# Optimization experiments

Hardware: AMD Instinct MI355X
Metric: run time of the kernel (lower is better)

Reference implementation:

```python
import jax, jax.numpy as jnp
import numpy as np
from jax import lax

B, S, D = 2, 2048, 1024
DS, K, L = 16, 4, 6
DI = 2 * D          # expand * d_model
V, A = 32000, 7
EPS = 1e-5


def setup_inputs() -> dict:
    key = jax.random.key(0)
    ks = jax.random.split(key, 20)
    g = lambda i, shape, s=0.02: (jax.random.normal(ks[i], shape, dtype=jnp.float32) * s)
    return {
        "features": jax.random.normal(ks[0], (B, S, D), dtype=jnp.float32),
        # per-layer Mamba params, stacked on leading layer dim
        "in_proj_w": g(1, (L, D, 2 * DI)),
        "conv_w": g(2, (L, DI, K), 0.1),
        "conv_b": g(3, (L, DI), 0.0),
        "B_ssm": g(4, (L, DI, DS)),   # fixed analogs of the per-step torch.randn(d_inner,d_state)
        "C_ssm": g(5, (L, DS, DI)),   # fixed analogs of the per-step torch.randn(d_state,d_inner)
        "out_w": g(6, (L, DI, D)),
        "ln_g": jnp.ones((D,), jnp.float32),
        "ln_b": jnp.zeros((D,), jnp.float32),
        # action head (arm: 7-dof, bounds (-1,1))
        "act_w1": g(7, (D, D // 2)), "act_b1": jnp.zeros((D // 2,), jnp.float32),
        "act_w2": g(8, (D // 2, D // 4)), "act_b2": jnp.zeros((D // 4,), jnp.float32),
        "act_w3": g(9, (D // 4, A)), "act_b3": jnp.zeros((A,), jnp.float32),
        # language head
        "lang_w1": g(10, (D, D)), "lang_b1": jnp.zeros((D,), jnp.float32),
        "lang_w2": g(11, (D, V)), "lang_b2": jnp.zeros((V,), jnp.float32),
    }


def _causal_dwconv(x, w, b):
    # x: [B,S,DI], w: [DI,K], b: [DI]  -> causal depthwise conv (torch pad=K-1 then trim)
    lhs = x.transpose(0, 2, 1)                    # [B,DI,S]
    rhs = w[:, None, :]                           # [DI,1,K]
    y = lax.conv_general_dilated(lhs, rhs, window_strides=(1,),
                                 padding=[(K - 1, 0)], feature_group_count=DI,
                                 dimension_numbers=("NCH", "OIH", "NCH"))
    return (y + b[None, :, None]).transpose(0, 2, 1)  # [B,S,DI]


def _selective_scan(xc, Bm, Cm):
    # xc: [B,S,DI]; h_t = 0.9*h_{t-1} + (x_t @ Bm)*0.1 ; y_t = h_t @ Cm
    u = jnp.einsum("bsi,in->bsn", xc, Bm) * 0.1      # [B,S,DS]
    def step(h, u_t):
        h = 0.9 * h + u_t
        return h, h
    _, hs = lax.scan(step, jnp.zeros((xc.shape[0], DS), xc.dtype), u.transpose(1, 0, 2))
    return jnp.einsum("sbn,ni->bsi", hs, Cm)         # [B,S,DI]


def _mamba_block(x, in_w, cw, cb, Bm, Cm, ow):
    xz = jnp.einsum("bsd,do->bso", x, in_w)          # [B,S,2*DI]
    xp, z = xz[..., :DI], xz[..., DI:]
    xc = jax.nn.silu(_causal_dwconv(xp, cw, cb))
    y = _selective_scan(xc, Bm, Cm) * jax.nn.silu(z)
    return jnp.einsum("bsi,id->bsd", y, ow)


def _forward(features, in_proj_w, conv_w, conv_b, B_ssm, C_ssm, out_w,
             ln_g, ln_b, act_w1, act_b1, act_w2, act_b2, act_w3, act_b3,
             lang_w1, lang_b1, lang_w2, lang_b2):
    x = features
    for l in range(L):  # residual Mamba layers (fallback path: x = x + block(x))
        x = x + _mamba_block(x, in_proj_w[l], conv_w[l], conv_b[l],
                             B_ssm[l], C_ssm[l], out_w[l])
    mu = jnp.mean(x, -1, keepdims=True)
    var = jnp.mean(jnp.square(x - mu), -1, keepdims=True)
    x = (x - mu) * lax.rsqrt(var + EPS) * ln_g + ln_b
    # action head: bounds (-1,1) => affine rescale is identity
    h = jax.nn.relu(x @ act_w1 + act_b1)
    h = jax.nn.relu(h @ act_w2 + act_b2)
    actions = jnp.tanh(h @ act_w3 + act_b3)
    # language head
    logits = jax.nn.relu(x @ lang_w1 + lang_b1) @ lang_w2 + lang_b2
    return actions, logits


def reference(features, in_proj_w, conv_w, conv_b, B_ssm, C_ssm, out_w,
              ln_g, ln_b, act_w1, act_b1, act_w2, act_b2, act_w3, act_b3,
              lang_w1, lang_b1, lang_w2, lang_b2):
    return _forward(features, in_proj_w, conv_w, conv_b, B_ssm, C_ssm, out_w,
                    ln_g, ln_b, act_w1, act_b1, act_w2, act_b2, act_w3, act_b3,
                    lang_w1, lang_b1, lang_w2, lang_b2)
```

## Files before the change

kernel.cpp:

```cpp
#include <hip/hip_runtime.h>
#include <hip/hip_bf16.h>
#include <cstdint>
#include <cstddef>

#define TT 4096
#define SS 2048
#define DD 1024
#define DDI 2048
#define LL 6
#define VV 32000
#define AA 7

typedef __hip_bfloat16 bf16;
typedef __attribute__((ext_vector_type(8))) short bf16x8;
typedef __attribute__((ext_vector_type(4))) short bf16x4;
typedef __attribute__((ext_vector_type(4))) float f32x4;

typedef const __attribute__((address_space(1))) void* gas_ptr;
typedef __attribute__((address_space(3))) void* las_ptr;

static __device__ __forceinline__ float b2f(bf16 h) { return __bfloat162float(h); }
static __device__ __forceinline__ bf16 f2b(float f) { return __float2bfloat16(f); }
static __device__ __forceinline__ float bs2f(short x) {
    unsigned int u = ((unsigned int)(unsigned short)x) << 16;
    float f; __builtin_memcpy(&f, &u, 4); return f;
}
static __device__ __forceinline__ short f2bs(float f) {
    bf16 h = f2b(f); unsigned short us; __builtin_memcpy(&us, &h, 2); return (short)us;
}

#define SWZ(off) ((off) ^ ((((off) >> 7) & 3) << 4))

template<int EPI>
__global__ __launch_bounds__(512, 2)
void g8_k(const bf16* __restrict__ A, const bf16* __restrict__ Wt,
          int K, int mx, int out_ld,
          float* __restrict__ of32, bf16* __restrict__ ob16,
          const float* __restrict__ bias)
{
    extern __shared__ char lds[];
    const int nwg = gridDim.x;
    int l = blockIdx.x;
    if ((nwg & 7) == 0) l = (l & 7) * (nwg >> 3) + (l >> 3);
    const int row0 = (l % mx) * 256, col0 = (l / mx) * 256;

    const int tid = threadIdx.x, wid = tid >> 6, lane = tid & 63;
    const int wr = wid >> 2, wc = wid & 3;
    const int l15 = lane & 15, kq = lane >> 4;

    f32x4 acc[8][4];
#pragma unroll
    for (int m = 0; m < 8; ++m)
#pragma unroll
        for (int n = 0; n < 4; ++n) acc[m][n] = f32x4{0.f, 0.f, 0.f, 0.f};

    const int sr   = tid >> 2;
    const int colE = (((tid & 3) ^ ((tid >> 3) & 3)) * 8);
    const bf16* gA = A  + (size_t)(row0 + sr) * K + colE;
    const bf16* gB = Wt + (size_t)(col0 + sr) * K + colE;
    const int dst0 = tid * 16, dst1 = 8192 + tid * 16;

    auto stageA = [&](int kh) {
        char* b = lds + (kh & 3) * 16384;
        __builtin_amdgcn_global_load_lds((gas_ptr)(gA + kh * 32),                   (las_ptr)(b + dst0), 16, 0, 0);
        __builtin_amdgcn_global_load_lds((gas_ptr)(gA + (size_t)128 * K + kh * 32), (las_ptr)(b + dst1), 16, 0, 0);
    };
    auto stageB = [&](int kh) {
        char* b = lds + 65536 + (kh & 3) * 16384;
        __builtin_amdgcn_global_load_lds((gas_ptr)(gB + kh * 32),                   (las_ptr)(b + dst0), 16, 0, 0);
        __builtin_amdgcn_global_load_lds((gas_ptr)(gB + (size_t)128 * K + kh * 32), (las_ptr)(b + dst1), 16, 0, 0);
    };

    const int NT = K >> 6, KH = K >> 5;
    stageA(0); stageB(0); stageA(1); stageB(1);
    stageA(2); stageB(2); stageA(3); stageB(3);
    int nextA = 4, nextB = 4;

    for (int t = 0; t < NT; ++t) {
        const char* As0 = lds + ((2 * t) & 3) * 16384;
        const char* As1 = lds + ((2 * t + 1) & 3) * 16384;
        const char* Bs0 = lds + 65536 + ((2 * t) & 3) * 16384;
        const char* Bs1 = lds + 65536 + ((2 * t + 1) & 3) * 16384;
        bf16x8 af[4], bfg[4];

        if (t < NT - 3) asm volatile("s_waitcnt vmcnt(10)" ::: "memory");
        else            asm volatile("s_waitcnt vmcnt(0)" ::: "memory");
        __builtin_amdgcn_sched_barrier(0);
        __builtin_amdgcn_s_barrier();
        __builtin_amdgcn_sched_barrier(0);
#pragma unroll
        for (int fn = 0; fn < 4; ++fn)
            bfg[fn] = *(const bf16x8*)(Bs0 + SWZ((wc * 64 + fn * 16 + l15) * 64 + kq * 16));
#pragma unroll
        for (int fm = 0; fm < 4; ++fm)
            af[fm] = *(const bf16x8*)(As0 + SWZ((wr * 128 + fm * 16 + l15) * 64 + kq * 16));
        if (t > 0 && nextA < KH) { stageA(nextA); ++nextA; }
        asm volatile("s_waitcnt lgkmcnt(0)" ::: "memory");
        __builtin_amdgcn_sched_barrier(0);
        __builtin_amdgcn_s_setprio(1);
#pragma unroll
        for (int fm = 0; fm < 4; ++fm)
#pragma unroll
            for (int fn = 0; fn < 4; ++fn)
                acc[fm][fn] = __builtin_amdgcn_mfma_f32_16x16x32_bf16(af[fm], bfg[fn], acc[fm][fn], 0, 0, 0);
        __builtin_amdgcn_s_setprio(0);
        __builtin_amdgcn_sched_barrier(0);
        __builtin_amdgcn_s_barrier();
        __builtin_amdgcn_sched_barrier(0);

#pragma unroll
        for (int fm = 0; fm < 4; ++fm)
            af[fm] = *(const bf16x8*)(As0 + SWZ((wr * 128 + 64 + fm * 16 + l15) * 64 + kq * 16));
        if (nextB < KH) { stageB(nextB); ++nextB; }
        asm volatile("s_waitcnt lgkmcnt(0)" ::: "memory");
        __builtin_amdgcn_sched_barrier(0);
        __builtin_amdgcn_s_setprio(1);
#pragma unroll
        for (int fm = 0; fm < 4; ++fm)
#pragma unroll
            for (int fn = 0; fn < 4; ++fn)
                acc[4 + fm][fn] = __builtin_amdgcn_mfma_f32_16x16x32_bf16(af[fm], bfg[fn], acc[4 + fm][fn], 0, 0, 0);
        __builtin_amdgcn_s_setprio(0);
        __builtin_amdgcn_sched_barrier(0);
        __builtin_amdgcn_s_barrier();
        __builtin_amdgcn_sched_barrier(0);

        if (t < NT - 3) asm volatile("s_waitcnt vmcnt(10)" ::: "memory");
        else            asm volatile("s_waitcnt vmcnt(0)" ::: "memory");
        __builtin_amdgcn_sched_barrier(0);
        __builtin_amdgcn_s_barrier();
        __builtin_amdgcn_sched_barrier(0);
#pragma unroll
        for (int fn = 0; fn < 4; ++fn)
            bfg[fn] = *(const bf16x8*)(Bs1 + SWZ((wc * 64 + fn * 16 + l15) * 64 + kq * 16));
#pragma unroll
        for (int fm = 0; fm < 4; ++fm)
            af[fm] = *(const bf16x8*)(As1 + SWZ((wr * 128 + fm * 16 + l15) * 64 + kq * 16));
        if (nextA < KH) { stageA(nextA); ++nextA; }
        asm volatile("s_waitcnt lgkmcnt(0)" ::: "memory");
        __builtin_amdgcn_sched_barrier(0);
        __builtin_amdgcn_s_setprio(1);
#pragma unroll
        for (int fm = 0; fm < 4; ++fm)
#pragma unroll
            for (int fn = 0; fn < 4; ++fn)
                acc[fm][fn] = __builtin_amdgcn_mfma_f32_16x16x32_bf16(af[fm], bfg[fn], acc[fm][fn], 0, 0, 0);
        __builtin_amdgcn_s_setprio(0);
        __builtin_amdgcn_sched_barrier(0);
        __builtin_amdgcn_s_barrier();
        __builtin_amdgcn_sched_barrier(0);

#pragma unroll
        for (int fm = 0; fm < 4; ++fm)
            af[fm] = *(const bf16x8*)(As1 + SWZ((wr * 128 + 64 + fm * 16 + l15) * 64 + kq * 16));
        if (nextB < KH) { stageB(nextB); ++nextB; }
        asm volatile("s_waitcnt lgkmcnt(0)" ::: "memory");
        __builtin_amdgcn_sched_barrier(0);
        __builtin_amdgcn_s_setprio(1);
#pragma unroll
        for (int fm = 0; fm < 4; ++fm)
#pragma unroll
            for (int fn = 0; fn < 4; ++fn)
                acc[4 + fm][fn] = __builtin_amdgcn_mfma_f32_16x16x32_bf16(af[fm], bfg[fn], acc[4 + fm][fn], 0, 0, 0);
        __builtin_amdgcn_s_setprio(0);
        __builtin_amdgcn_sched_barrier(0);
        __builtin_amdgcn_s_barrier();
        __builtin_amdgcn_sched_barrier(0);
    }

    float* sc = (float*)(lds + wid * 16384);
#pragma unroll
    for (int h = 0; h < 2; ++h) {
        asm volatile("s_waitcnt lgkmcnt(0)" ::: "memory");
        __builtin_amdgcn_sched_barrier(0);
#pragma unroll
        for (int fm = 0; fm < 4; ++fm)
#pragma unroll
            for (int fn = 0; fn < 4; ++fn)
#pragma unroll
                for (int r = 0; r < 4; ++r)
                    sc[(fm * 16 + kq * 4 + r) * 64 + fn * 16 + l15] = acc[h * 4 + fm][fn][r];
        asm volatile("s_waitcnt lgkmcnt(0)" ::: "memory");
        __builtin_amdgcn_sched_barrier(0);
#pragma unroll
        for (int j = 0; j < 16; ++j) {
            const int rl = j * 4 + kq;
            f32x4 v4 = *(const f32x4*)&sc[rl * 64 + l15 * 4];
            const int row = row0 + wr * 128 + h * 64 + rl;
            const int col = col0 + wc * 64 + l15 * 4;
            if (EPI == 0) {
                bf16x4 ov = { f2bs(v4[0]), f2bs(v4[1]), f2bs(v4[2]), f2bs(v4[3]) };
                *(bf16x4*)(ob16 + (size_t)row * out_ld + col) = ov;
            } else {
                float4 bv = *(const float4*)(bias + col);
                f32x4 ov = { v4[0] + bv.x, v4[1] + bv.y, v4[2] + bv.z, v4[3] + bv.w };
                *(f32x4*)(of32 + (size_t)row * out_ld + col) = ov;
            }
        }
    }
}

template<int EPI>
__global__ __launch_bounds__(256, 2)
void g8h_k(const bf16* __restrict__ A, const bf16* __restrict__ Wt,
           int K, int mx, int out_ld,
           float* __restrict__ of32, bf16* __restrict__ ob16,
           const float* __restrict__ bias)
{
    extern __shared__ char lds[];
    const int nwg = gridDim.x;
    int l = blockIdx.x;
    if ((nwg & 7) == 0) l = (l & 7) * (nwg >> 3) + (l >> 3);
    const int row0 = (l % mx) * 128, col0 = (l / mx) * 128;

    const int tid = threadIdx.x, wid = tid >> 6, lane = tid & 63;
    const int wr = wid >> 1, wc = wid & 1;
    const int l15 = lane & 15, kq = lane >> 4;

    f32x4 acc[4][4];
#pragma unroll
    for (int m = 0; m < 4; ++m)
#pragma unroll
        for (int n = 0; n < 4; ++n) acc[m][n] = f32x4{0.f, 0.f, 0.f, 0.f};

    const int sr   = tid >> 2;
    const int colE = (((tid & 3) ^ ((tid >> 3) & 3)) * 8);
    const bf16* gA = A  + (size_t)(row0 + sr) * K + colE;
    const bf16* gB = Wt + (size_t)(col0 + sr) * K + colE;
    const int dst0 = tid * 16, dst1 = 4096 + tid * 16;

    auto stage = [&](int kh) {
        char* a = lds + (kh % 5) * 8192;
        char* b = lds + 40960 + (kh % 5) * 8192;
        __builtin_amdgcn_global_load_lds((gas_ptr)(gA + kh * 32),                  (las_ptr)(a + dst0), 16, 0, 0);
        __builtin_amdgcn_global_load_lds((gas_ptr)(gA + (size_t)64 * K + kh * 32), (las_ptr)(a + dst1), 16, 0, 0);
        __builtin_amdgcn_global_load_lds((gas_ptr)(gB + kh * 32),                  (las_ptr)(b + dst0), 16, 0, 0);
        __builtin_amdgcn_global_load_lds((gas_ptr)(gB + (size_t)64 * K + kh * 32), (las_ptr)(b + dst1), 16, 0, 0);
    };

    const int KH = K >> 5;
    stage(0); stage(1); stage(2); stage(3);

    for (int kh = 0; kh < KH; ++kh) {
        const int rem = KH - 1 - kh;
        if (rem >= 3)      asm volatile("s_waitcnt vmcnt(12)" ::: "memory");
        else if (rem == 2) asm volatile("s_waitcnt vmcnt(8)" ::: "memory");
        else if (rem == 1) asm volatile("s_waitcnt vmcnt(4)" ::: "memory");
        else               asm volatile("s_waitcnt vmcnt(0)" ::: "memory");
        __builtin_amdgcn_sched_barrier(0);
        __builtin_amdgcn_s_barrier();
        __builtin_amdgcn_sched_barrier(0);

        const char* As = lds + (kh % 5) * 8192;
        const char* Bs = lds + 40960 + (kh % 5) * 8192;
        bf16x8 af[4], bfg[4];
#pragma unroll
        for (int fn = 0; fn < 4; ++fn)
            bfg[fn] = *(const bf16x8*)(Bs + SWZ((wc * 64 + fn * 16 + l15) * 64 + kq * 16));
#pragma unroll
        for (int fm = 0; fm < 4; ++fm)
            af[fm] = *(const bf16x8*)(As + SWZ((wr * 64 + fm * 16 + l15) * 64 + kq * 16));
        if (kh + 4 < KH) stage(kh + 4);
        asm volatile("s_waitcnt lgkmcnt(0)" ::: "memory");
        __builtin_amdgcn_sched_barrier(0);
        __builtin_amdgcn_s_setprio(1);
#pragma unroll
        for (int fm = 0; fm < 4; ++fm)
#pragma unroll
            for (int fn = 0; fn < 4; ++fn)
                acc[fm][fn] = __builtin_amdgcn_mfma_f32_16x16x32_bf16(af[fm], bfg[fn], acc[fm][fn], 0, 0, 0);
        __builtin_amdgcn_s_setprio(0);
        __builtin_amdgcn_sched_barrier(0);
    }

#pragma unroll
    for (int fm = 0; fm < 4; ++fm) {
#pragma unroll
        for (int fn = 0; fn < 4; ++fn) {
#pragma unroll
            for (int r = 0; r < 4; ++r) {
                const int row = row0 + wr * 64 + fm * 16 + kq * 4 + r;
                const int col = col0 + wc * 64 + fn * 16 + l15;
                float v = acc[fm][fn][r];
                if (EPI == 3) {
                    float rr = of32[(size_t)row * out_ld + col] + v;
                    of32[(size_t)row * out_ld + col] = rr;
                    ob16[(size_t)row * out_ld + col] = f2b(rr);
                } else {
                    ob16[(size_t)row * out_ld + col] = f2b(v);
                }
            }
        }
    }
}

template<int EPI>
__global__ __launch_bounds__(256)
void gemm_k(const bf16* __restrict__ A, const bf16* __restrict__ Wt,
            int K, int out_ld,
            float* __restrict__ of32, bf16* __restrict__ ob16,
            const float* __restrict__ bias)
{
    __shared__ bf16x8 lsA8[128 * 4];
    __shared__ bf16x8 lsB8[128 * 4];
    bf16* lsA = (bf16*)lsA8;
    bf16* lsB = (bf16*)lsB8;

    const int tid  = threadIdx.x;
    const int w    = tid >> 6;
    const int lane = tid & 63;
    const int row0 = blockIdx.x * 128;
    const int col0 = blockIdx.y * 128;
    const int wr   = (w >> 1) * 64;
    const int wc   = (w & 1) * 64;
    const int l15  = lane & 15;
    const int kq   = lane >> 4;

    f32x4 acc[4][4];
#pragma unroll
    for (int m = 0; m < 4; ++m)
#pragma unroll
        for (int n = 0; n < 4; ++n) acc[m][n] = f32x4{0.f, 0.f, 0.f, 0.f};

    const int s0 = tid, s1 = tid + 256;
    const size_t ga0 = (size_t)(row0 + (s0 >> 2)) * K + (s0 & 3) * 8;
    const size_t ga1 = (size_t)(row0 + (s1 >> 2)) * K + (s1 & 3) * 8;
    const size_t gb0 = (size_t)(col0 + (s0 >> 2)) * K + (s0 & 3) * 8;
    const size_t gb1 = (size_t)(col0 + (s1 >> 2)) * K + (s1 & 3) * 8;
    bf16* la0 = lsA + (size_t)(w * 64) * 8;
    bf16* la1 = lsA + (size_t)(256 + w * 64) * 8;
    bf16* lb0 = lsB + (size_t)(w * 64) * 8;
    bf16* lb1 = lsB + (size_t)(256 + w * 64) * 8;

    for (int k0 = 0; k0 < K; k0 += 32) {
        __builtin_amdgcn_global_load_lds((gas_ptr)(A  + ga0 + k0), (las_ptr)la0, 16, 0, 0);
        __builtin_amdgcn_global_load_lds((gas_ptr)(A  + ga1 + k0), (las_ptr)la1, 16, 0, 0);
        __builtin_amdgcn_global_load_lds((gas_ptr)(Wt + gb0 + k0), (las_ptr)lb0, 16, 0, 0);
        __builtin_amdgcn_global_load_lds((gas_ptr)(Wt + gb1 + k0), (las_ptr)lb1, 16, 0, 0);
        __syncthreads();

        bf16x8 af[4], bfr[4];
#pragma unroll
        for (int m = 0; m < 4; ++m)
            af[m] = *(const bf16x8*)(lsA + (size_t)(wr + m * 16 + l15) * 32 + kq * 8);
#pragma unroll
        for (int n = 0; n < 4; ++n)
            bfr[n] = *(const bf16x8*)(lsB + (size_t)(wc + n * 16 + l15) * 32 + kq * 8);
#pragma unroll
        for (int m = 0; m < 4; ++m)
#pragma unroll
            for (int n = 0; n < 4; ++n)
                acc[m][n] = __builtin_amdgcn_mfma_f32_16x16x32_bf16(af[m], bfr[n], acc[m][n], 0, 0, 0);
        __syncthreads();
    }

#pragma unroll
    for (int m = 0; m < 4; ++m) {
#pragma unroll
        for (int n = 0; n < 4; ++n) {
#pragma unroll
            for (int r = 0; r < 4; ++r) {
                const int row = row0 + wr + m * 16 + kq * 4 + r;
                const int col = col0 + wc + n * 16 + l15;
                float v = acc[m][n][r];
                v = fmaxf(v + bias[col], 0.f);
                ob16[(size_t)row * out_ld + col] = f2b(v);
            }
        }
    }
}

__global__ __launch_bounds__(256)
void cusk_k(const bf16* __restrict__ xz, const float* __restrict__ cw,
            const float* __restrict__ cb, const bf16* __restrict__ Wt,
            float* __restrict__ up)
{
    __shared__ bf16x8 lsA8[128 * 4];
    __shared__ bf16x8 lsB8[128 * 4];
    bf16* lsA = (bf16*)lsA8;
    bf16* lsB = (bf16*)lsB8;
    const int K = 2048;

    const int tid  = threadIdx.x;
    const int w    = tid >> 6;
    const int lane = tid & 63;
    const int row0 = blockIdx.x * 128;
    const int spl  = blockIdx.y;
    const int kbeg = spl * 256;
    const int wr   = (w >> 1) * 64;
    const int wc   = (w & 1) * 64;
    const int l15  = lane & 15;
    const int kq   = lane >> 4;

    f32x4 acc[4][4];
#pragma unroll
    for (int m = 0; m < 4; ++m)
#pragma unroll
        for (int n = 0; n < 4; ++n) acc[m][n] = f32x4{0.f, 0.f, 0.f, 0.f};

    const int trow = tid >> 2, tch = tid & 3;
    const int r0g = row0 + trow, r1g = r0g + 64;
    const int sq0 = r0g & (SS - 1), sq1 = r1g & (SS - 1);

    const int s0 = tid, s1 = tid + 256;
    const size_t gb0 = (size_t)(s0 >> 2) * K + (s0 & 3) * 8;
    const size_t gb1 = (size_t)(s1 >> 2) * K + (s1 & 3) * 8;
    bf16* lb0 = lsB + (size_t)(w * 64) * 8;
    bf16* lb1 = lsB + (size_t)(256 + w * 64) * 8;

    for (int k0 = kbeg; k0 < kbeg + 256; k0 += 32) {
        const int i0 = k0 + tch * 8;

        __builtin_amdgcn_global_load_lds((gas_ptr)(Wt + gb0 + k0), (las_ptr)lb0, 16, 0, 0);
        __builtin_amdgcn_global_load_lds((gas_ptr)(Wt + gb1 + k0), (las_ptr)lb1, 16, 0, 0);

        bf16x8 vA0, vA1;
        {
            const bf16* b0 = xz + (size_t)r0g * 4096 + i0;
            bf16x8 x0 = *(const bf16x8*)b0;
            bf16x8 x1 = {}, x2 = {}, x3 = {};
            if (sq0 >= 1) x1 = *(const bf16x8*)(b0 - 4096);
            if (sq0 >= 2) x2 = *(const bf16x8*)(b0 - 2 * 4096);
            if (sq0 >= 3) x3 = *(const bf16x8*)(b0 - 3 * 4096);
#pragma unroll
            for (int c = 0; c < 8; ++c) {
                float4 wv4 = ((const float4*)cw)[i0 + c];
                float a = cb[i0 + c];
                a = fmaf(bs2f(x3[c]), wv4.x, a);
                a = fmaf(bs2f(x2[c]), wv4.y, a);
                a = fmaf(bs2f(x1[c]), wv4.z, a);
                a = fmaf(bs2f(x0[c]), wv4.w, a);
                float sig = 1.f / (1.f + expf(-a));
                vA0[c] = f2bs(a * sig);
            }
        }
        {
            const bf16* b0 = xz + (size_t)r1g * 4096 + i0;
            bf16x8 x0 = *(const bf16x8*)b0;
            bf16x8 x1 = {}, x2 = {}, x3 = {};
            if (sq1 >= 1) x1 = *(const bf16x8*)(b0 - 4096);
            if (sq1 >= 2) x2 = *(const bf16x8*)(b0 - 2 * 4096);
            if (sq1 >= 3) x3 = *(const bf16x8*)(b0 - 3 * 4096);
#pragma unroll
            for (int c = 0; c < 8; ++c) {
                float4 wv4 = ((const float4*)cw)[i0 + c];
                float a = cb[i0 + c];
                a = fmaf(bs2f(x3[c]), wv4.x, a);
                a = fmaf(bs2f(x2[c]), wv4.y, a);
                a = fmaf(bs2f(x1[c]), wv4.z, a);
                a = fmaf(bs2f(x0[c]), wv4.w, a);
                float sig = 1.f / (1.f + expf(-a));
                vA1[c] = f2bs(a * sig);
            }
        }
        lsA8[tid] = vA0;
        lsA8[tid + 256] = vA1;
        __syncthreads();

        bf16x8 af[4], bfr[4];
#pragma unroll
        for (int m = 0; m < 4; ++m)
            af[m] = *(const bf16x8*)(lsA + (size_t)(wr + m * 16 + l15) * 32 + kq * 8);
#pragma unroll
        for (int n = 0; n < 4; ++n)
            bfr[n] = *(const bf16x8*)(lsB + (size_t)(wc + n * 16 + l15) * 32 + kq * 8);
#pragma unroll
        for (int m = 0; m < 4; ++m)
#pragma unroll
            for (int n = 0; n < 4; ++n)
                acc[m][n] = __builtin_amdgcn_mfma_f32_16x16x32_bf16(af[m], bfr[n], acc[m][n], 0, 0, 0);
        __syncthreads();
    }

    if (wc == 0) {
#pragma unroll
        for (int m = 0; m < 4; ++m)
#pragma unroll
            for (int r = 0; r < 4; ++r) {
                const int row = row0 + wr + m * 16 + kq * 4 + r;
                up[(size_t)spl * TT * 16 + (size_t)row * 16 + l15] = acc[m][0][r];
            }
    }
}

__global__ void ured_k(const float* __restrict__ up, float* __restrict__ u)
{
    int i = blockIdx.x * 256 + threadIdx.x;
    float s = 0.f;
#pragma unroll
    for (int k = 0; k < 8; ++k) s += up[(size_t)k * TT * 16 + i];
    u[i] = s;
}

__global__ __launch_bounds__(256)
void transpose_k(const float* __restrict__ W, bf16* __restrict__ WT, int K, int N)
{
    __shared__ bf16 t[64][66];
    const int k0 = blockIdx.x * 64, n0 = blockIdx.y * 64;
    const int tid = threadIdx.x;
#pragma unroll
    for (int i = 0; i < 16; ++i) {
        int idx = i * 256 + tid;
        int kk = idx >> 6, nn = idx & 63;
        t[nn][kk] = f2b(W[(size_t)(k0 + kk) * N + n0 + nn]);
    }
    __syncthreads();
#pragma unroll
    for (int i = 0; i < 16; ++i) {
        int idx = i * 256 + tid;
        int nn = idx >> 6, kk = idx & 63;
        WT[(size_t)(n0 + nn) * K + k0 + kk] = t[nn][kk];
    }
}

__global__ void prep_bm_k(const float* __restrict__ Bm, bf16* __restrict__ BmT)
{
    int idx = blockIdx.x * 256 + threadIdx.x;
    int n = idx >> 11, k = idx & 2047;
    float v = (n < 16) ? Bm[(size_t)k * 16 + n] * 0.1f : 0.f;
    BmT[idx] = f2b(v);
}

__global__ void copyfeat_k(const float* __restrict__ f, float* __restrict__ xf,
                           bf16* __restrict__ xb)
{
    int i = (blockIdx.x * 256 + threadIdx.x) * 4;
    float4 v = *(const float4*)(f + i);
    *(float4*)(xf + i) = v;
    xb[i + 0] = f2b(v.x);
    xb[i + 1] = f2b(v.y);
    xb[i + 2] = f2b(v.z);
    xb[i + 3] = f2b(v.w);
}

__global__ void scan2_k(const float* __restrict__ u, float* __restrict__ hs)
{
    int gid = blockIdx.x * 256 + threadIdx.x;
    int n = gid & 15, c = (gid >> 4) & 63, b = gid >> 10;
    int start = c * 32;
    const float* ub = u + (size_t)b * SS * 16;
    float* hb = hs + (size_t)b * SS * 16;
    float h = 0.f;
    int w0 = start - 96; if (w0 < 0) w0 = 0;
    for (int t = w0; t < start; ++t) h = 0.9f * h + ub[(size_t)t * 16 + n];
    for (int t = start; t < start + 32; ++t) {
        h = 0.9f * h + ub[(size_t)t * 16 + n];
        hb[(size_t)t * 16 + n] = h;
    }
}

__global__ __launch_bounds__(256)
void yk_k(const float* __restrict__ hs, const float* __restrict__ Cm,
          const bf16* __restrict__ xz, bf16* __restrict__ y)
{
    const int t = blockIdx.x, i0 = threadIdx.x * 8;
    const float* h = hs + (size_t)t * 16;
    float o[8] = {0.f, 0.f, 0.f, 0.f, 0.f, 0.f, 0.f, 0.f};
#pragma unroll
    for (int n = 0; n < 16; ++n) {
        float hn = h[n];
        const float4* c = (const float4*)(Cm + (size_t)n * DDI + i0);
        float4 c0 = c[0], c1 = c[1];
        o[0] = fmaf(hn, c0.x, o[0]); o[1] = fmaf(hn, c0.y, o[1]);
        o[2] = fmaf(hn, c0.z, o[2]); o[3] = fmaf(hn, c0.w, o[3]);
        o[4] = fmaf(hn, c1.x, o[4]); o[5] = fmaf(hn, c1.y, o[5]);
        o[6] = fmaf(hn, c1.z, o[6]); o[7] = fmaf(hn, c1.w, o[7]);
    }
    bf16x8 zv = *(const bf16x8*)(xz + (size_t)t * 4096 + 2048 + i0);
    bf16* yo = y + (size_t)t * DDI + i0;
#pragma unroll
    for (int j = 0; j < 8; ++j) {
        float zf = bs2f(zv[j]);
        yo[j] = f2b(o[j] * (zf / (1.f + expf(-zf))));
    }
}

__global__ __launch_bounds__(256)
void ln_k(const float* __restrict__ x, const float* __restrict__ g,
          const float* __restrict__ bb, bf16* __restrict__ xn)
{
    int t = blockIdx.x, tid = threadIdx.x;
    const float* xr = x + (size_t)t * DD;
    float4 v = *(const float4*)(xr + tid * 4);
    float s = v.x + v.y + v.z + v.w;
#pragma unroll
    for (int o = 32; o > 0; o >>= 1) s += __shfl_down(s, o, 64);
    __shared__ float r1[4], r2[4];
    if ((tid & 63) == 0) r1[tid >> 6] = s;
    __syncthreads();
    float mu = (r1[0] + r1[1] + r1[2] + r1[3]) * (1.f / DD);
    float d0 = v.x - mu, d1 = v.y - mu, d2 = v.z - mu, d3 = v.w - mu;
    float ss = d0 * d0 + d1 * d1 + d2 * d2 + d3 * d3;
#pragma unroll
    for (int o = 32; o > 0; o >>= 1) ss += __shfl_down(ss, o, 64);
    if ((tid & 63) == 0) r2[tid >> 6] = ss;
    __syncthreads();
    float var = (r2[0] + r2[1] + r2[2] + r2[3]) * (1.f / DD);
    float inv = rsqrtf(var + 1e-5f);
    int di = tid * 4;
    xn[(size_t)t * DD + di + 0] = f2b(d0 * inv * g[di + 0] + bb[di + 0]);
    xn[(size_t)t * DD + di + 1] = f2b(d1 * inv * g[di + 1] + bb[di + 1]);
    xn[(size_t)t * DD + di + 2] = f2b(d2 * inv * g[di + 2] + bb[di + 2]);
    xn[(size_t)t * DD + di + 3] = f2b(d3 * inv * g[di + 3] + bb[di + 3]);
}

__global__ void act3_k(const bf16* __restrict__ h2, const float* __restrict__ w3,
                       const float* __restrict__ b3, float* __restrict__ out)
{
    int idx = blockIdx.x * 256 + threadIdx.x;
    if (idx >= TT * AA) return;
    int t = idx / AA, a = idx - t * AA;
    float acc = b3[a];
    const bf16* hr = h2 + (size_t)t * 256;
    for (int k = 0; k < 256; ++k)
        acc = fmaf(b2f(hr[k]), w3[k * AA + a], acc);
    out[idx] = tanhf(acc);
}

extern "C" void kernel_launch(void* const* d_in, const int* in_sizes, int n_in,
                              void* d_out, int out_size, void* d_ws, size_t ws_size,
                              hipStream_t stream)
{
    (void)in_sizes; (void)n_in; (void)out_size; (void)ws_size;
    const float* features = (const float*)d_in[0];
    const float* in_proj_w = (const float*)d_in[1];
    const float* conv_w = (const float*)d_in[2];
    const float* conv_b = (const float*)d_in[3];
    const float* B_ssm = (const float*)d_in[4];
    const float* C_ssm = (const float*)d_in[5];
    const float* out_w = (const float*)d_in[6];
    const float* ln_g = (const float*)d_in[7];
    const float* ln_b = (const float*)d_in[8];
    const float* act_w1 = (const float*)d_in[9];
    const float* act_b1 = (const float*)d_in[10];
    const float* act_w2 = (const float*)d_in[11];
    const float* act_b2 = (const float*)d_in[12];
    const float* act_w3 = (const float*)d_in[13];
    const float* act_b3 = (const float*)d_in[14];
    const float* lang_w1 = (const float*)d_in[15];
    const float* lang_b1 = (const float*)d_in[16];
    const float* lang_w2 = (const float*)d_in[17];
    const float* lang_b2 = (const float*)d_in[18];

    static bool attr_done = false;
    if (!attr_done) {
        hipFuncSetAttribute((const void*)&g8_k<0>, hipFuncAttributeMaxDynamicSharedMemorySize, 131072);
        hipFuncSetAttribute((const void*)&g8_k<5>, hipFuncAttributeMaxDynamicSharedMemorySize, 131072);
        hipFuncSetAttribute((const void*)&g8h_k<3>, hipFuncAttributeMaxDynamicSharedMemorySize, 81920);
        attr_done = true;
    }

    char* p = (char*)d_ws;
    size_t off = 0;
    auto alloc = [&](size_t bytes) -> void* {
        void* q = p + off;
        off = (off + bytes + 255) & ~(size_t)255;
        return q;
    };
    float* x_f  = (float*)alloc((size_t)TT * DD * 4);
    bf16*  x_b  = (bf16*) alloc((size_t)TT * DD * 2);
    bf16*  xz   = (bf16*) alloc((size_t)TT * 4096 * 2);
    bf16*  y    = (bf16*) alloc((size_t)TT * DDI * 2);
    float* u    = (float*)alloc((size_t)TT * 16 * 4);
    float* up   = (float*)alloc((size_t)8 * TT * 16 * 4);
    float* hs   = (float*)alloc((size_t)TT * 16 * 4);
    bf16*  xn   = (bf16*) alloc((size_t)TT * DD * 2);
    bf16*  h1   = (bf16*) alloc((size_t)TT * 512 * 2);
    bf16*  h2   = (bf16*) alloc((size_t)TT * 256 * 2);
    bf16*  hl   = (bf16*) alloc((size_t)TT * DD * 2);
    bf16*  inwT = (bf16*) alloc((size_t)LL * 4096 * 1024 * 2);
    bf16*  owT  = (bf16*) alloc((size_t)LL * 1024 * 2048 * 2);
    bf16*  bmT  = (bf16*) alloc((size_t)LL * 128 * 2048 * 2);
    bf16*  a1T  = (bf16*) alloc((size_t)512 * 1024 * 2);
    bf16*  a2T  = (bf16*) alloc((size_t)256 * 512 * 2);
    bf16*  l1T  = (bf16*) alloc((size_t)1024 * 1024 * 2);
    bf16*  l2T  = (bf16*) alloc((size_t)VV * 1024 * 2);

    copyfeat_k<<<TT * DD / 1024, 256, 0, stream>>>(features, x_f, x_b);
    for (int l = 0; l < LL; ++l) {
        transpose_k<<<dim3(16, 64), 256, 0, stream>>>(in_proj_w + (size_t)l * 1024 * 4096,
                                                      inwT + (size_t)l * 4096 * 1024, 1024, 4096);
        transpose_k<<<dim3(32, 16), 256, 0, stream>>>(out_w + (size_t)l * 2048 * 1024,
                                                      owT + (size_t)l * 1024 * 2048, 2048, 1024);
        prep_bm_k<<<(128 * 2048) / 256, 256, 0, stream>>>(B_ssm + (size_t)l * 2048 * 16,
                                                          bmT + (size_t)l * 128 * 2048);
    }
    transpose_k<<<dim3(16, 8), 256, 0, stream>>>(act_w1, a1T, 1024, 512);
    transpose_k<<<dim3(8, 4), 256, 0, stream>>>(act_w2, a2T, 512, 256);
    transpose_k<<<dim3(16, 16), 256, 0, stream>>>(lang_w1, l1T, 1024, 1024);
    transpose_k<<<dim3(16, 500), 256, 0, stream>>>(lang_w2, l2T, 1024, VV);

    for (int l = 0; l < LL; ++l) {
        g8_k<0><<<256, 512, 131072, stream>>>(x_b, inwT + (size_t)l * 4096 * 1024,
                                              1024, 16, 4096, nullptr, xz, nullptr);
        cusk_k<<<dim3(32, 8), 256, 0, stream>>>(xz, conv_w + (size_t)l * DDI * 4,
                                                conv_b + (size_t)l * DDI,
                                                bmT + (size_t)l * 128 * 2048, up);
        ured_k<<<TT * 16 / 256, 256, 0, stream>>>(up, u);
        scan2_k<<<8, 256, 0, stream>>>(u, hs);
        yk_k<<<TT, 256, 0, stream>>>(hs, C_ssm + (size_t)l * 16 * 2048, xz, y);
        g8h_k<3><<<256, 256, 81920, stream>>>(y, owT + (size_t)l * 1024 * 2048,
                                              2048, 32, 1024, x_f, x_b, nullptr);
    }

    ln_k<<<TT, 256, 0, stream>>>(x_f, ln_g, ln_b, xn);
    gemm_k<4><<<dim3(32, 4), 256, 0, stream>>>(xn, a1T, 1024, 512, nullptr, h1, act_b1);
    gemm_k<4><<<dim3(32, 2), 256, 0, stream>>>(h1, a2T, 512, 256, nullptr, h2, act_b2);
    act3_k<<<(TT * AA + 255) / 256, 256, 0, stream>>>(h2, act_w3, act_b3, (float*)d_out);
    gemm_k<4><<<dim3(32, 8), 256, 0, stream>>>(xn, l1T, 1024, 1024, nullptr, hl, lang_b1);
    g8_k<5><<<2000, 512, 131072, stream>>>(hl, l2T, 1024, 16, VV,
                                           (float*)d_out + (size_t)TT * AA, nullptr, lang_b2);
}
```

Baseline: 1.598 ms.

## Use 128x256 tiled in_proj GEMM with triple-buffered LDS pipeline

Replaces the 256x256-tile in_proj GEMM with a new kernel using 128x256 tiles, a 32-wide K step, and a three-stage global_load_lds ring buffer in static LDS. This doubles the grid to 512 workgroups so more CUs stay busy on the 4096x4096x1024 GEMM, and uses a smaller LDS footprint. The trade-off is less operand reuse per tile, more barriers per K, and scalar bf16 output stores.

```diff
diff --git a/kernel.cpp b/kernel.cpp
--- a/kernel.cpp
+++ b/kernel.cpp
@@ -30,6 +30,86 @@
 }
 
 #define SWZ(off) ((off) ^ ((((off) >> 7) & 3) << 4))
+
+__global__ __launch_bounds__(512, 2)
+void g8w_k(const bf16* __restrict__ A, const bf16* __restrict__ Wt,
+           int K, int mx, int out_ld, bf16* __restrict__ ob16)
+{
+    __shared__ char lds[73728];
+    const int nwg = gridDim.x;
+    int l = blockIdx.x;
+    if ((nwg & 7) == 0) l = (l & 7) * (nwg >> 3) + (l >> 3);
+    const int row0 = (l % mx) * 128, col0 = (l / mx) * 256;
+
+    const int tid = threadIdx.x, wid = tid >> 6, lane = tid & 63;
+    const int wr = wid >> 2, wc = wid & 3;
+    const int l15 = lane & 15, kq = lane >> 4;
+
+    f32x4 acc[4][4];
+#pragma unroll
+    for (int m = 0; m < 4; ++m)
+#pragma unroll
+        for (int n = 0; n < 4; ++n) acc[m][n] = f32x4{0.f, 0.f, 0.f, 0.f};
+
+    const int sr   = tid >> 2;
+    const int colE = (((tid & 3) ^ ((tid >> 3) & 3)) * 8);
+    const bf16* gA = A  + (size_t)(row0 + sr) * K + colE;
+    const bf16* gB = Wt + (size_t)(col0 + sr) * K + colE;
+    const int dst = tid * 16;
+
+    auto stage = [&](int kh) {
+        char* a = lds + (kh % 3) * 8192;
+        char* b = lds + 24576 + (kh % 3) * 16384;
+        __builtin_amdgcn_global_load_lds((gas_ptr)(gA + kh * 32),                   (las_ptr)(a + dst), 16, 0, 0);
+        __builtin_amdgcn_global_load_lds((gas_ptr)(gB + kh * 32),                   (las_ptr)(b + dst), 16, 0, 0);
+        __builtin_amdgcn_global_load_lds((gas_ptr)(gB + (size_t)128 * K + kh * 32), (las_ptr)(b + 8192 + dst), 16, 0, 0);
+    };
+
+    const int KH = K >> 5;
+    stage(0); stage(1);
+
+    for (int kh = 0; kh < KH; ++kh) {
+        if (kh < KH - 1) asm volatile("s_waitcnt vmcnt(3)" ::: "memory");
+        else             asm volatile("s_waitcnt vmcnt(0)" ::: "memory");
+        __builtin_amdgcn_sched_barrier(0);
+        __builtin_amdgcn_s_barrier();
+        __builtin_amdgcn_sched_barrier(0);
+
+        const char* As = lds + (kh % 3) * 8192;
+        const char* Bs = lds + 24576 + (kh % 3) * 16384;
+        bf16x8 af[4], bfg[4];
+#pragma unroll
+        for (int fn = 0; fn < 4; ++fn)
+            bfg[fn] = *(const bf16x8*)(Bs + SWZ((wc * 64 + fn * 16 + l15) * 64 + kq * 16));
+#pragma unroll
+        for (int fm = 0; fm < 4; ++fm)
+            af[fm] = *(const bf16x8*)(As + SWZ((wr * 64 + fm * 16 + l15) * 64 + kq * 16));
+        if (kh + 2 < KH) stage(kh + 2);
+        asm volatile("s_waitcnt lgkmcnt(0)" ::: "memory");
+        __builtin_amdgcn_sched_barrier(0);
+        __builtin_amdgcn_s_setprio(1);
+#pragma unroll
+        for (int fm = 0; fm < 4; ++fm)
+#pragma unroll
+            for (int fn = 0; fn < 4; ++fn)
+                acc[fm][fn] = __builtin_amdgcn_mfma_f32_16x16x32_bf16(af[fm], bfg[fn], acc[fm][fn], 0, 0, 0);
+        __builtin_amdgcn_s_setprio(0);
+        __builtin_amdgcn_sched_barrier(0);
+    }
+
+#pragma unroll
+    for (int fm = 0; fm < 4; ++fm) {
+#pragma unroll
+        for (int fn = 0; fn < 4; ++fn) {
+#pragma unroll
+            for (int r = 0; r < 4; ++r) {
+                const int row = row0 + wr * 64 + fm * 16 + kq * 4 + r;
+                const int col = col0 + wc * 64 + fn * 16 + l15;
+                ob16[(size_t)row * out_ld + col] = f2b(acc[fm][fn][r]);
+            }
+        }
+    }
+}
 
 template<int EPI>
 __global__ __launch_bounds__(512, 2)
@@ -644,7 +724,6 @@
 
     static bool attr_done = false;
     if (!attr_done) {
-        hipFuncSetAttribute((const void*)&g8_k<0>, hipFuncAttributeMaxDynamicSharedMemorySize, 131072);
         hipFuncSetAttribute((const void*)&g8_k<5>, hipFuncAttributeMaxDynamicSharedMemorySize, 131072);
         hipFuncSetAttribute((const void*)&g8h_k<3>, hipFuncAttributeMaxDynamicSharedMemorySize, 81920);
         attr_done = true;
@@ -691,8 +770,8 @@
     transpose_k<<<dim3(16, 500), 256, 0, stream>>>(lang_w2, l2T, 1024, VV);
 
     for (int l = 0; l < LL; ++l) {
-        g8_k<0><<<256, 512, 131072, stream>>>(x_b, inwT + (size_t)l * 4096 * 1024,
-                                              1024, 16, 4096, nullptr, xz, nullptr);
+        g8w_k<<<512, 512, 0, stream>>>(x_b, inwT + (size_t)l * 4096 * 1024,
+                                       1024, 32, 4096, xz);
         cusk_k<<<dim3(32, 8), 256, 0, stream>>>(xz, conv_w + (size_t)l * DDI * 4,
                                                 conv_b + (size_t)l * DDI,
                                                 bmT + (size_t)l * 128 * 2048, up);
```

New measurement: 1.630 ms. Within noise of the previous version (+2.0%).
